# Kernel tuning notes

Hardware: AMD Instinct MI355X
Metric: run time of the kernel (lower is better)

## Reference

```python
import math
import jax, jax.numpy as jnp
import numpy as np

BS, NTOK, NHEADS, WIDTH, WIN = 2, 4096, 8, 32, 32


def _make_coo():
    d = np.repeat(np.arange(NTOK), WIN)
    j = np.tile(np.arange(WIN), NTOK)
    s = (d + j) % NTOK
    # dst_cnt = j (dense per-dst counter), src_cnt = j (dense per-src counter,
    # since for fixed src the contributing dsts have distinct j)
    return jnp.asarray(np.stack([d, s, j, j], axis=1), dtype=jnp.int32)


def setup_inputs() -> dict:
    key = jax.random.key(0)
    k1, k2, k3, k4 = jax.random.split(key, 4)
    shape = (BS, NTOK, NHEADS, WIDTH)
    return {
        "vf": jax.random.normal(k1, shape, dtype=jnp.float32),
        "vb": jax.random.normal(k2, shape, dtype=jnp.float32),
        "q": jax.random.normal(k3, shape, dtype=jnp.float32),
        "k": jax.random.normal(k4, shape, dtype=jnp.float32),
        "coo": _make_coo(),
        "dst_mxlen": WIN,
        "src_mxlen": WIN,
        "use_softmax": 1,
    }


def reference(vf, vb, q, k, coo, dst_mxlen, src_mxlen, use_softmax):
    # q,k,vf,vb: [bs, n_tok, n_heads, width]; coo: [cl,4] = [dst,src,dst_cnt,src_cnt]
    # COO formulation equivalent to the torch padded-dense buffers: padded slots
    # carry exp(-1e12)=0, sentinel column adds exp(0)=1 to each softmax denominator.
    dst, src = coo[:, 0], coo[:, 1]
    n_tok, width = q.shape[1], q.shape[3]
    scale = -1.0 / math.sqrt(width)
    # L1 attention scores per COO entry -> [cl, bs, h]
    ww = (jnp.sum(jnp.abs(q[:, dst] - k[:, src]), axis=-1) * scale).transpose(1, 0, 2)
    if use_softmax:
        # softmax per dst over its entries plus a zero sentinel slot
        m = jnp.maximum(jax.ops.segment_max(ww, dst, num_segments=n_tok), 0.0)  # [n_tok,bs,h]
        e = jnp.exp(ww - m[dst])
        denom = jax.ops.segment_sum(e, dst, num_segments=n_tok) + jnp.exp(-m)
        attn = e / denom[dst]  # [cl, bs, h]
    else:
        attn = jnp.exp(ww)
    # forward aggregation: per dst, weighted sum of vf[src]
    vfo = jax.ops.segment_sum(attn[..., None] * vf[:, src].transpose(1, 0, 2, 3),
                              dst, num_segments=n_tok)  # [n_tok, bs, h, w]
    # backward aggregation: per src, same weights applied to vb[dst]
    vbo = jax.ops.segment_sum(attn[..., None] * vb[:, dst].transpose(1, 0, 2, 3),
                              src, num_segments=n_tok)  # [n_tok, bs, h, w]
    return (vfo + vbo).transpose(1, 0, 2, 3)  # [bs, n_tok, h, w]
```

## Files before the change

kernel.cpp:

```cpp
#include <hip/hip_runtime.h>
#include <math.h>

#define BS 2
#define NTOK 4096
#define NMASK 4095
#define NHEADS 8
#define WIN 32
#define HALO 31
#define RA 95
#define RK 127
#define NTILES 64
#define SCALE (-0.17677669529663687f)

using u32 = unsigned int;
using h2 = __attribute__((ext_vector_type(2))) _Float16;
using h4 = __attribute__((ext_vector_type(4))) _Float16;
using f32x4 = __attribute__((ext_vector_type(4))) float;

static __device__ __forceinline__ u32 packrtz(float x, float y) {
  auto p = __builtin_amdgcn_cvt_pkrtz(x, y);
  return __builtin_bit_cast(u32, p);
}
static __device__ __forceinline__ uint4 pack8(float4 a, float4 b) {
  return make_uint4(packrtz(a.x, a.y), packrtz(a.z, a.w), packrtz(b.x, b.y),
                    packrtz(b.z, b.w));
}
static __device__ __forceinline__ h2 habs(h2 v) {
  return __builtin_bit_cast(h2, __builtin_bit_cast(u32, v) & 0x7fff7fffu);
}
static __device__ __forceinline__ float dot2acc(h2 a, float acc) {
#if __has_builtin(__builtin_amdgcn_fdot2)
  const h2 one = {(_Float16)1.f, (_Float16)1.f};
  return __builtin_amdgcn_fdot2(a, one, acc, false);
#else
  return acc + (float)a[0] + (float)a[1];
#endif
}

template <int CTRL>
static __device__ __forceinline__ float dppadd(float v) {
  int y = __builtin_amdgcn_update_dpp(0, __builtin_bit_cast(int, v), CTRL,
                                      0xF, 0xF, true);
  return v + __builtin_bit_cast(float, y);
}
static __device__ __forceinline__ float sum32(float v) {
  v = dppadd<0xB1>(v);
  v = dppadd<0x4E>(v);
  v = dppadd<0x141>(v);
  v = dppadd<0x140>(v);
  v += __shfl_xor(v, 16, 32);
  return v;
}

static __device__ __forceinline__ void lds_barrier() {
  asm volatile("s_waitcnt lgkmcnt(0)\n\ts_barrier" ::: "memory");
}

__global__ __launch_bounds__(256) void l1attn_fused(
    const float* __restrict__ q, const float* __restrict__ k,
    const float* __restrict__ vf, const float* __restrict__ vb,
    float* __restrict__ out, const int* __restrict__ use_sm_p) {
  const int tid = threadIdx.x;
  const int g = blockIdx.x;
  const int tile = g & (NTILES - 1);
  const int bh = g >> 6;
  const int h = bh & (NHEADS - 1);
  const int b = bh >> 3;
  const int t0 = tile << 6;

  const size_t base4 = ((size_t)b * NTOK) * 64 + (size_t)h * 8;
  const float4* qg = (const float4*)q;
  const float4* kg = (const float4*)k;
  const float4* vfg = (const float4*)vf;
  const float4* vbg = (const float4*)vb;

  __shared__ uint4 k_s[4 * 128];
  __shared__ uint4 q_s[4 * 96];
  __shared__ u32 vf_c[32 * 52];
  __shared__ u32 vb_c[32 * 52];
  __shared__ __align__(8) _Float16 atf[64 * 48];
  __shared__ __align__(8) _Float16 atb[64 * 52];

  const int kr0 = tid >> 2, km0 = tid & 3;
  const float4* kp0 =
      kg + base4 + (size_t)((t0 - HALO + kr0) & NMASK) * 64 + 2 * km0;
  float4 ka0 = kp0[0], ka1 = kp0[1];
  const bool has_k1 = tid < RK * 4 - 256;
  const int kr1 = (tid + 256) >> 2, km1 = (tid + 256) & 3;
  float4 kb0, kb1;
  if (has_k1) {
    const float4* kp1 =
        kg + base4 + (size_t)((t0 - HALO + kr1) & NMASK) * 64 + 2 * km1;
    kb0 = kp1[0];
    kb1 = kp1[1];
  }
  const int qr0 = tid >> 2, qm0 = tid & 3;
  const float4* qp0 =
      qg + base4 + (size_t)((t0 - HALO + qr0) & NMASK) * 64 + 2 * qm0;
  float4 qa0 = qp0[0], qa1 = qp0[1];
  const bool has_q1 = tid < 128;
  const int qr1 = (tid + 256) >> 2, qm1 = (tid + 256) & 3;
  float4 qb0, qb1;
  if (has_q1) {
    const float4* qp1 =
        qg + base4 + (size_t)((t0 - HALO + qr1) & NMASK) * 64 + 2 * qm1;
    qb0 = qp1[0];
    qb1 = qp1[1];
  }
  const int rp0 = tid >> 3, c0 = tid & 7;
  float4 f00 = vfg[base4 + (size_t)((t0 + 2 * rp0) & NMASK) * 64 + c0];
  float4 f01 = vfg[base4 + (size_t)((t0 + 2 * rp0 + 1) & NMASK) * 64 + c0];
  float4 g00 = vbg[base4 + (size_t)((t0 - HALO + 2 * rp0) & NMASK) * 64 + c0];
  float4 g01 =
      vbg[base4 + (size_t)((t0 - HALO + 2 * rp0 + 1) & NMASK) * 64 + c0];
  const int rp1 = (tid + 256) >> 3, c1 = (tid + 256) & 7;
  float4 f10, f11, g10, g11;
  if (has_q1) {
    f10 = vfg[base4 + (size_t)((t0 + 2 * rp1) & NMASK) * 64 + c1];
    f11 = vfg[base4 + (size_t)((t0 + 2 * rp1 + 1) & NMASK) * 64 + c1];
    g10 = vbg[base4 + (size_t)((t0 - HALO + 2 * rp1) & NMASK) * 64 + c1];
    g11 = vbg[base4 + (size_t)((t0 - HALO + 2 * rp1 + 1) & NMASK) * 64 + c1];
  }

  k_s[km0 * 128 + kr0] = pack8(ka0, ka1);
  if (has_k1) k_s[km1 * 128 + kr1] = pack8(kb0, kb1);
  q_s[qm0 * 96 + qr0] = pack8(qa0, qa1);
  if (has_q1) q_s[qm1 * 96 + qr1] = pack8(qb0, qb1);
  {
    u32* az = (u32*)atf;
    for (int i = tid; i < 1536; i += 256) az[i] = 0;
    u32* bz = (u32*)atb;
    for (int i = tid; i < 1664; i += 256) bz[i] = 0;
  }
  lds_barrier();

  {
    const int lane = tid & 63, wid = tid >> 6;
    const int hh = lane >> 5, j = lane & 31;
    const int use_sm = *use_sm_p;
    const int row0 = wid * 24 + hh;

#pragma unroll
    for (int it = 0; it < 12; ++it) {
      const int row = row0 + it * 2;
      if (row < RA) {
        const int kr = row + j;
        float acc = 0.f;
#pragma unroll
        for (int m = 0; m < 4; ++m) {
          uint4 qq = q_s[m * 96 + row];
          uint4 kk = k_s[m * 128 + kr];
          acc = dot2acc(habs(__builtin_bit_cast(h2, qq.x) -
                             __builtin_bit_cast(h2, kk.x)), acc);
          acc = dot2acc(habs(__builtin_bit_cast(h2, qq.y) -
                             __builtin_bit_cast(h2, kk.y)), acc);
          acc = dot2acc(habs(__builtin_bit_cast(h2, qq.z) -
                             __builtin_bit_cast(h2, kk.z)), acc);
          acc = dot2acc(habs(__builtin_bit_cast(h2, qq.w) -
                             __builtin_bit_cast(h2, kk.w)), acc);
        }
        float e = __expf(acc * SCALE);
        float att;
        if (use_sm) {
          float s = sum32(e);
          att = e * __builtin_amdgcn_rcpf(1.f + s);
        } else {
          att = e;
        }
        _Float16 a16 = (_Float16)att;
        if (row >= HALO) {
          int tl = row - HALO;
          atf[tl * 48 + (tl & 15) + j] = a16;
        }
        int tl2 = row + j - HALO;
        if ((unsigned)tl2 < 64u) {
          atb[tl2 * 52 + (tl2 & 15) + 31 - j] = a16;
        }
      }
    }
  }

  vf_c[(4 * c0 + 0) * 52 + rp0] = packrtz(f00.x, f01.x);
  vf_c[(4 * c0 + 1) * 52 + rp0] = packrtz(f00.y, f01.y);
  vf_c[(4 * c0 + 2) * 52 + rp0] = packrtz(f00.z, f01.z);
  vf_c[(4 * c0 + 3) * 52 + rp0] = packrtz(f00.w, f01.w);
  vb_c[(4 * c0 + 0) * 52 + rp0] = packrtz(g00.x, g01.x);
  vb_c[(4 * c0 + 1) * 52 + rp0] = packrtz(g00.y, g01.y);
  vb_c[(4 * c0 + 2) * 52 + rp0] = packrtz(g00.z, g01.z);
  vb_c[(4 * c0 + 3) * 52 + rp0] = packrtz(g00.w, g01.w);
  if (has_q1) {
    vf_c[(4 * c1 + 0) * 52 + rp1] = packrtz(f10.x, f11.x);
    vf_c[(4 * c1 + 1) * 52 + rp1] = packrtz(f10.y, f11.y);
    vf_c[(4 * c1 + 2) * 52 + rp1] = packrtz(f10.z, f11.z);
    vf_c[(4 * c1 + 3) * 52 + rp1] = packrtz(f10.w, f11.w);
    vb_c[(4 * c1 + 0) * 52 + rp1] = packrtz(g10.x, g11.x);
    vb_c[(4 * c1 + 1) * 52 + rp1] = packrtz(g10.y, g11.y);
    vb_c[(4 * c1 + 2) * 52 + rp1] = packrtz(g10.z, g11.z);
    vb_c[(4 * c1 + 3) * 52 + rp1] = packrtz(g10.w, g11.w);
  }
  lds_barrier();

  {
    const int l = tid & 63, wid = tid >> 6;
    const int r16 = l & 15, k4 = l >> 4;
    const _Float16* vfh = (const _Float16*)vf_c;
    const _Float16* vbh = (const _Float16*)vb_c;

    h4 afr[3], abr[3];
#pragma unroll
    for (int kt = 0; kt < 3; ++kt) {
      afr[kt] = *(const h4*)(atf + (wid * 16 + r16) * 48 + 16 * kt + 4 * k4);
      abr[kt] = *(const h4*)(atb + (wid * 16 + r16) * 52 + 16 * kt + 4 * k4);
    }
    const int kbase = 16 * wid + 4 * k4;
#pragma unroll
    for (int nt = 0; nt < 2; ++nt) {
      const int col = nt * 16 + r16;
      f32x4 acc = {0.f, 0.f, 0.f, 0.f};
#if __has_builtin(__builtin_amdgcn_mfma_f32_16x16x16f16)
#pragma unroll
      for (int kt = 0; kt < 3; ++kt) {
        h4 bf = *(const h4*)(vfh + col * 104 + kbase + 16 * kt);
        acc = __builtin_amdgcn_mfma_f32_16x16x16f16(afr[kt], bf, acc, 0, 0, 0);
      }
#pragma unroll
      for (int kt = 0; kt < 3; ++kt) {
        h4 bb = *(const h4*)(vbh + col * 104 + kbase + 16 * kt);
        acc = __builtin_amdgcn_mfma_f32_16x16x16f16(abr[kt], bb, acc, 0, 0, 0);
      }
#else
#pragma unroll
      for (int reg = 0; reg < 4; ++reg) {
        float s = 0.f;
        int mrow = 4 * k4 + reg;
        for (int kk = 0; kk < 48; ++kk) {
          s += (float)atf[(wid * 16 + mrow) * 48 + kk] *
                   (float)vfh[col * 104 + 16 * wid + kk] +
               (float)atb[(wid * 16 + mrow) * 52 + kk] *
                   (float)vbh[col * 104 + 16 * wid + kk];
        }
        acc[reg] = s;
      }
#endif
      const int t = t0 + 16 * wid + 4 * k4;
      const size_t ob =
          ((size_t)b * NTOK) * 256 + (size_t)t * 256 + h * 32 + col;
      out[ob] = acc[0];
      out[ob + 256] = acc[1];
      out[ob + 512] = acc[2];
      out[ob + 768] = acc[3];
    }
  }
}

extern "C" void kernel_launch(void* const* d_in, const int* in_sizes, int n_in,
                              void* d_out, int out_size, void* d_ws,
                              size_t ws_size, hipStream_t stream) {
  const float* vf = (const float*)d_in[0];
  const float* vb = (const float*)d_in[1];
  const float* q = (const float*)d_in[2];
  const float* k = (const float*)d_in[3];
  const int* use_sm = (const int*)d_in[7];
  float* out = (float*)d_out;

  const int blocks = BS * NHEADS * NTILES;
  l1attn_fused<<<blocks, 256, 0, stream>>>(q, k, vf, vb, out, use_sm);
}
```

Before: 22.24 us.

## Halve token tile to 32 and alias shared memory for more blocks

Shrinks each block's token tile from 64 to 32, doubling the grid to 2048 blocks. Shared buffers are unioned into one aliased region so K/Q staging is reused for V storage, which needs an extra barrier. Each wave now computes one 16x16 output tile instead of two. The aim is more blocks and higher occupancy from lower LDS use. The cost is relatively more halo recompute and halo loads per output token.

```diff
diff --git a/kernel.cpp b/kernel.cpp
--- a/kernel.cpp
+++ b/kernel.cpp
@@ -7,9 +7,9 @@
 #define NHEADS 8
 #define WIN 32
 #define HALO 31
-#define RA 95
-#define RK 127
-#define NTILES 64
+#define RA 63
+#define RKROWS 94
+#define NTILES 128
 #define SCALE (-0.17677669529663687f)
 
 using u32 = unsigned int;
@@ -63,10 +63,10 @@
   const int tid = threadIdx.x;
   const int g = blockIdx.x;
   const int tile = g & (NTILES - 1);
-  const int bh = g >> 6;
+  const int bh = g >> 7;
   const int h = bh & (NHEADS - 1);
   const int b = bh >> 3;
-  const int t0 = tile << 6;
+  const int t0 = tile << 5;
 
   const size_t base4 = ((size_t)b * NTOK) * 64 + (size_t)h * 8;
   const float4* qg = (const float4*)q;
@@ -74,82 +74,65 @@
   const float4* vfg = (const float4*)vf;
   const float4* vbg = (const float4*)vb;
 
-  __shared__ uint4 k_s[4 * 128];
-  __shared__ uint4 q_s[4 * 96];
-  __shared__ u32 vf_c[32 * 52];
-  __shared__ u32 vb_c[32 * 52];
-  __shared__ __align__(8) _Float16 atf[64 * 48];
-  __shared__ __align__(8) _Float16 atb[64 * 52];
+  __shared__ __align__(16) char smem[16896];
+  uint4* k_s = (uint4*)smem;
+  uint4* q_s = (uint4*)(smem + 6144);
+  u32* vf_c = (u32*)smem;
+  u32* vb_c = (u32*)(smem + 4352);
+  _Float16* atf = (_Float16*)(smem + 10240);
+  _Float16* atb = (_Float16*)(smem + 13568);
 
   const int kr0 = tid >> 2, km0 = tid & 3;
   const float4* kp0 =
       kg + base4 + (size_t)((t0 - HALO + kr0) & NMASK) * 64 + 2 * km0;
   float4 ka0 = kp0[0], ka1 = kp0[1];
-  const bool has_k1 = tid < RK * 4 - 256;
-  const int kr1 = (tid + 256) >> 2, km1 = (tid + 256) & 3;
+  const bool has_k1 = tid < (RKROWS * 4 - 256);
+  const int kr1 = (tid + 256) >> 2;
   float4 kb0, kb1;
   if (has_k1) {
     const float4* kp1 =
-        kg + base4 + (size_t)((t0 - HALO + kr1) & NMASK) * 64 + 2 * km1;
+        kg + base4 + (size_t)((t0 - HALO + kr1) & NMASK) * 64 + 2 * km0;
     kb0 = kp1[0];
     kb1 = kp1[1];
   }
-  const int qr0 = tid >> 2, qm0 = tid & 3;
-  const float4* qp0 =
-      qg + base4 + (size_t)((t0 - HALO + qr0) & NMASK) * 64 + 2 * qm0;
-  float4 qa0 = qp0[0], qa1 = qp0[1];
-  const bool has_q1 = tid < 128;
-  const int qr1 = (tid + 256) >> 2, qm1 = (tid + 256) & 3;
-  float4 qb0, qb1;
-  if (has_q1) {
-    const float4* qp1 =
-        qg + base4 + (size_t)((t0 - HALO + qr1) & NMASK) * 64 + 2 * qm1;
-    qb0 = qp1[0];
-    qb1 = qp1[1];
+  const bool has_q = tid < RA * 4;
+  const int qr0 = tid >> 2;
+  float4 qa0, qa1;
+  if (has_q) {
+    const float4* qp0 =
+        qg + base4 + (size_t)((t0 - HALO + qr0) & NMASK) * 64 + 2 * km0;
+    qa0 = qp0[0];
+    qa1 = qp0[1];
   }
   const int rp0 = tid >> 3, c0 = tid & 7;
-  float4 f00 = vfg[base4 + (size_t)((t0 + 2 * rp0) & NMASK) * 64 + c0];
-  float4 f01 = vfg[base4 + (size_t)((t0 + 2 * rp0 + 1) & NMASK) * 64 + c0];
-  float4 g00 = vbg[base4 + (size_t)((t0 - HALO + 2 * rp0) & NMASK) * 64 + c0];
-  float4 g01 =
+  float4 f0 = vfg[base4 + (size_t)((t0 + 2 * rp0) & NMASK) * 64 + c0];
+  float4 f1 = vfg[base4 + (size_t)((t0 + 2 * rp0 + 1) & NMASK) * 64 + c0];
+  float4 g0 = vbg[base4 + (size_t)((t0 - HALO + 2 * rp0) & NMASK) * 64 + c0];
+  float4 g1 =
       vbg[base4 + (size_t)((t0 - HALO + 2 * rp0 + 1) & NMASK) * 64 + c0];
-  const int rp1 = (tid + 256) >> 3, c1 = (tid + 256) & 7;
-  float4 f10, f11, g10, g11;
-  if (has_q1) {
-    f10 = vfg[base4 + (size_t)((t0 + 2 * rp1) & NMASK) * 64 + c1];
-    f11 = vfg[base4 + (size_t)((t0 + 2 * rp1 + 1) & NMASK) * 64 + c1];
-    g10 = vbg[base4 + (size_t)((t0 - HALO + 2 * rp1) & NMASK) * 64 + c1];
-    g11 = vbg[base4 + (size_t)((t0 - HALO + 2 * rp1 + 1) & NMASK) * 64 + c1];
-  }
-
-  k_s[km0 * 128 + kr0] = pack8(ka0, ka1);
-  if (has_k1) k_s[km1 * 128 + kr1] = pack8(kb0, kb1);
-  q_s[qm0 * 96 + qr0] = pack8(qa0, qa1);
-  if (has_q1) q_s[qm1 * 96 + qr1] = pack8(qb0, qb1);
+
+  k_s[km0 * 96 + kr0] = pack8(ka0, ka1);
+  if (has_k1) k_s[km0 * 96 + kr1] = pack8(kb0, kb1);
+  if (has_q) q_s[km0 * 64 + qr0] = pack8(qa0, qa1);
   {
-    u32* az = (u32*)atf;
-    for (int i = tid; i < 1536; i += 256) az[i] = 0;
-    u32* bz = (u32*)atb;
-    for (int i = tid; i < 1664; i += 256) bz[i] = 0;
+    u32* z = (u32*)atf;
+    for (int i = tid; i < 1664; i += 256) z[i] = 0;
   }
   lds_barrier();
 
   {
-    const int lane = tid & 63, wid = tid >> 6;
-    const int hh = lane >> 5, j = lane & 31;
+    const int grp = tid >> 5, j = tid & 31;
     const int use_sm = *use_sm_p;
-    const int row0 = wid * 24 + hh;
-
-#pragma unroll
-    for (int it = 0; it < 12; ++it) {
-      const int row = row0 + it * 2;
+#pragma unroll
+    for (int it = 0; it < 8; ++it) {
+      const int row = grp * 8 + it;
       if (row < RA) {
         const int kr = row + j;
         float acc = 0.f;
 #pragma unroll
         for (int m = 0; m < 4; ++m) {
-          uint4 qq = q_s[m * 96 + row];
-          uint4 kk = k_s[m * 128 + kr];
+          uint4 qq = q_s[m * 64 + row];
+          uint4 kk = k_s[m * 96 + kr];
           acc = dot2acc(habs(__builtin_bit_cast(h2, qq.x) -
                              __builtin_bit_cast(h2, kk.x)), acc);
           acc = dot2acc(habs(__builtin_bit_cast(h2, qq.y) -
@@ -170,38 +153,30 @@
         _Float16 a16 = (_Float16)att;
         if (row >= HALO) {
           int tl = row - HALO;
-          atf[tl * 48 + (tl & 15) + j] = a16;
+          atf[tl * 52 + (tl & 15) + j] = a16;
         }
         int tl2 = row + j - HALO;
-        if ((unsigned)tl2 < 64u) {
+        if ((unsigned)tl2 < 32u) {
           atb[tl2 * 52 + (tl2 & 15) + 31 - j] = a16;
         }
       }
     }
   }
-
-  vf_c[(4 * c0 + 0) * 52 + rp0] = packrtz(f00.x, f01.x);
-  vf_c[(4 * c0 + 1) * 52 + rp0] = packrtz(f00.y, f01.y);
-  vf_c[(4 * c0 + 2) * 52 + rp0] = packrtz(f00.z, f01.z);
-  vf_c[(4 * c0 + 3) * 52 + rp0] = packrtz(f00.w, f01.w);
-  vb_c[(4 * c0 + 0) * 52 + rp0] = packrtz(g00.x, g01.x);
-  vb_c[(4 * c0 + 1) * 52 + rp0] = packrtz(g00.y, g01.y);
-  vb_c[(4 * c0 + 2) * 52 + rp0] = packrtz(g00.z, g01.z);
-  vb_c[(4 * c0 + 3) * 52 + rp0] = packrtz(g00.w, g01.w);
-  if (has_q1) {
-    vf_c[(4 * c1 + 0) * 52 + rp1] = packrtz(f10.x, f11.x);
-    vf_c[(4 * c1 + 1) * 52 + rp1] = packrtz(f10.y, f11.y);
-    vf_c[(4 * c1 + 2) * 52 + rp1] = packrtz(f10.z, f11.z);
-    vf_c[(4 * c1 + 3) * 52 + rp1] = packrtz(f10.w, f11.w);
-    vb_c[(4 * c1 + 0) * 52 + rp1] = packrtz(g10.x, g11.x);
-    vb_c[(4 * c1 + 1) * 52 + rp1] = packrtz(g10.y, g11.y);
-    vb_c[(4 * c1 + 2) * 52 + rp1] = packrtz(g10.z, g11.z);
-    vb_c[(4 * c1 + 3) * 52 + rp1] = packrtz(g10.w, g11.w);
-  }
+  lds_barrier();
+
+  vf_c[(4 * c0 + 0) * 34 + rp0] = packrtz(f0.x, f1.x);
+  vf_c[(4 * c0 + 1) * 34 + rp0] = packrtz(f0.y, f1.y);
+  vf_c[(4 * c0 + 2) * 34 + rp0] = packrtz(f0.z, f1.z);
+  vf_c[(4 * c0 + 3) * 34 + rp0] = packrtz(f0.w, f1.w);
+  vb_c[(4 * c0 + 0) * 34 + rp0] = packrtz(g0.x, g1.x);
+  vb_c[(4 * c0 + 1) * 34 + rp0] = packrtz(g0.y, g1.y);
+  vb_c[(4 * c0 + 2) * 34 + rp0] = packrtz(g0.z, g1.z);
+  vb_c[(4 * c0 + 3) * 34 + rp0] = packrtz(g0.w, g1.w);
   lds_barrier();
 
   {
     const int l = tid & 63, wid = tid >> 6;
+    const int mt = wid >> 1, nt = wid & 1;
     const int r16 = l & 15, k4 = l >> 4;
     const _Float16* vfh = (const _Float16*)vf_c;
     const _Float16* vbh = (const _Float16*)vb_c;
@@ -209,47 +184,44 @@
     h4 afr[3], abr[3];
 #pragma unroll
     for (int kt = 0; kt < 3; ++kt) {
-      afr[kt] = *(const h4*)(atf + (wid * 16 + r16) * 48 + 16 * kt + 4 * k4);
-      abr[kt] = *(const h4*)(atb + (wid * 16 + r16) * 52 + 16 * kt + 4 * k4);
-    }
-    const int kbase = 16 * wid + 4 * k4;
-#pragma unroll
-    for (int nt = 0; nt < 2; ++nt) {
-      const int col = nt * 16 + r16;
-      f32x4 acc = {0.f, 0.f, 0.f, 0.f};
+      afr[kt] = *(const h4*)(atf + (mt * 16 + r16) * 52 + 16 * kt + 4 * k4);
+      abr[kt] = *(const h4*)(atb + (mt * 16 + r16) * 52 + 16 * kt + 4 * k4);
+    }
+    const int kbase = 16 * mt + 4 * k4;
+    const int col = nt * 16 + r16;
+    f32x4 acc = {0.f, 0.f, 0.f, 0.f};
 #if __has_builtin(__builtin_amdgcn_mfma_f32_16x16x16f16)
 #pragma unroll
-      for (int kt = 0; kt < 3; ++kt) {
-        h4 bf = *(const h4*)(vfh + col * 104 + kbase + 16 * kt);
-        acc = __builtin_amdgcn_mfma_f32_16x16x16f16(afr[kt], bf, acc, 0, 0, 0);
+    for (int kt = 0; kt < 3; ++kt) {
+      h4 bf = *(const h4*)(vfh + col * 68 + kbase + 16 * kt);
+      acc = __builtin_amdgcn_mfma_f32_16x16x16f16(afr[kt], bf, acc, 0, 0, 0);
+    }
+#pragma unroll
+    for (int kt = 0; kt < 3; ++kt) {
+      h4 bb = *(const h4*)(vbh + col * 68 + kbase + 16 * kt);
+      acc = __builtin_amdgcn_mfma_f32_16x16x16f16(abr[kt], bb, acc, 0, 0, 0);
+    }
+#else
+#pragma unroll
+    for (int reg = 0; reg < 4; ++reg) {
+      float s = 0.f;
+      int mrow = 4 * k4 + reg;
+      for (int kk = 0; kk < 48; ++kk) {
+        s += (float)atf[(mt * 16 + mrow) * 52 + kk] *
+                 (float)vfh[col * 68 + 16 * mt + kk] +
+             (float)atb[(mt * 16 + mrow) * 52 + kk] *
+                 (float)vbh[col * 68 + 16 * mt + kk];
       }
-#pragma unroll
-      for (int kt = 0; kt < 3; ++kt) {
-        h4 bb = *(const h4*)(vbh + col * 104 + kbase + 16 * kt);
-        acc = __builtin_amdgcn_mfma_f32_16x16x16f16(abr[kt], bb, acc, 0, 0, 0);
-      }
-#else
-#pragma unroll
-      for (int reg = 0; reg < 4; ++reg) {
-        float s = 0.f;
-        int mrow = 4 * k4 + reg;
-        for (int kk = 0; kk < 48; ++kk) {
-          s += (float)atf[(wid * 16 + mrow) * 48 + kk] *
-                   (float)vfh[col * 104 + 16 * wid + kk] +
-               (float)atb[(wid * 16 + mrow) * 52 + kk] *
-                   (float)vbh[col * 104 + 16 * wid + kk];
-        }
-        acc[reg] = s;
-      }
+      acc[reg] = s;
+    }
 #endif
-      const int t = t0 + 16 * wid + 4 * k4;
-      const size_t ob =
-          ((size_t)b * NTOK) * 256 + (size_t)t * 256 + h * 32 + col;
-      out[ob] = acc[0];
-      out[ob + 256] = acc[1];
-      out[ob + 512] = acc[2];
-      out[ob + 768] = acc[3];
-    }
+    const int t = t0 + 16 * mt + 4 * k4;
+    const size_t ob =
+        ((size_t)b * NTOK) * 256 + (size_t)t * 256 + h * 32 + col;
+    out[ob] = acc[0];
+    out[ob + 256] = acc[1];
+    out[ob + 512] = acc[2];
+    out[ob + 768] = acc[3];
   }
 }
 
```

Result: no change. 22.66 us (+1.9%).
